# Kernel tuning notes

Measured on AMD Instinct MI355X. Metric: run time of the kernel, lower is better.

The kernel has to match this reference:

```python
import jax, jax.numpy as jnp
import numpy as np

N = 100000   # num_nodes
E = 3200000  # num_edges (avg degree 32)
T = 16       # channels
L = 2        # n_layers


def setup_inputs() -> dict:
    key = jax.random.key(0)
    ks = jax.random.split(key, 6)
    x = jax.random.normal(ks[0], (T, N), dtype=jnp.float32)
    edge_index = jax.random.randint(ks[1], (2, E), 0, N)
    # per-layer scalar params (shared='all' -> shape [1,1] each), init U(-1,1)
    alpha1 = jax.random.uniform(ks[2], (L, 1, 1), minval=-1.0, maxval=1.0, dtype=jnp.float32)
    alpha2 = jax.random.uniform(ks[3], (L, 1, 1), minval=-1.0, maxval=1.0, dtype=jnp.float32)
    gamma = jax.random.uniform(ks[4], (L, 1, 1), minval=-1.0, maxval=1.0, dtype=jnp.float32)
    bias = jax.random.uniform(ks[5], (L, 1, 1), minval=-1.0, maxval=1.0, dtype=jnp.float32)
    return {"x": x, "edge_index": edge_index, "alpha1": alpha1,
            "alpha2": alpha2, "gamma": gamma, "bias": bias}


def reference(x, edge_index, alpha1, alpha2, gamma, bias):
    # DGMRF forward (transpose=False, with_bias=True): stack of L DGMRFLayerMultiChannel
    src, dst = edge_index[0], edge_index[1]
    # degrees = ptg.utils.degree(edge_index[0]) (out-degree of source nodes)
    deg = jax.ops.segment_sum(jnp.ones(E, dtype=x.dtype), src, num_segments=N)
    log_deg = jnp.log(deg)[None, :]          # [1, N]
    edge_log_deg = log_deg[0, dst][None, :]  # [1, E] = log_degrees[edge_index[1]] (non-transpose)
    for l in range(L):
        dp = jax.nn.sigmoid(gamma[l])        # degree_power, [1,1]
        sw = jnp.exp(alpha1[l])              # self_weight
        # NOTE: source's alpha2 property returns alpha1_param when shared != 'dynamics'
        nw = sw * jnp.tanh(alpha1[l])        # neighbor_weight
        weighted_repr = x * jnp.exp(dp * log_deg)        # [T, N]
        ew = jnp.exp((dp - 1.0) * edge_log_deg)          # [1, E] (base edge_weights are ones)
        msg = x[:, src] * ew                              # gather + weight: [T, E]
        agg = jnp.zeros_like(x).at[:, dst].add(msg)       # scatter-add aggregate
        x = sw * weighted_repr + nw * agg + bias[l]
    return x
```

## Files before the change

kernel.cpp:

```cpp
#include <hip/hip_runtime.h>


#define TCH 16
#define BBITS 8
#define BINW (1 << BBITS)
#define BLK 256

typedef int   v4i __attribute__((ext_vector_type(4)));
typedef int   v2i __attribute__((ext_vector_type(2)));
typedef float v4f __attribute__((ext_vector_type(4)));
typedef unsigned int v2u __attribute__((ext_vector_type(2)));

__device__ __forceinline__ float4 bf4_to_f4(uint2 v) {
    float4 f;
    f.x = __uint_as_float(v.x << 16);
    f.y = __uint_as_float(v.x & 0xFFFF0000u);
    f.z = __uint_as_float(v.y << 16);
    f.w = __uint_as_float(v.y & 0xFFFF0000u);
    return f;
}
__device__ __forceinline__ unsigned rne_bf16(float f) {
    unsigned u = __float_as_uint(f);
    return (u + 0x7FFFu + ((u >> 16) & 1u)) >> 16;
}
__device__ __forceinline__ unsigned pack_bf2(float a, float b) {
    return rne_bf16(a) | (rne_bf16(b) << 16);
}

__global__ void k_histtin(const int* __restrict__ src, const int* __restrict__ dst,
                          int* __restrict__ Hd, int* __restrict__ Hs,
                          const float* __restrict__ x, float* __restrict__ xtf,
                          unsigned short* __restrict__ xtb,
                          int E, int N, int NB, int CHUNK, int NBLK) {
    extern __shared__ int sm[];
    int* cd = sm; int* cs2 = sm + NB;
    int t = threadIdx.x;
    if (blockIdx.x < (unsigned)NBLK) {
        for (int i = t; i < 2 * NB; i += BLK) sm[i] = 0;
        __syncthreads();
        int beg = blockIdx.x * CHUNK;
        int end = beg + CHUNK; if (end > E) end = E;
        for (int i = beg + t; i < end; i += BLK) {
            atomicAdd(&cd[dst[i] >> BBITS], 1);
            atomicAdd(&cs2[src[i] >> BBITS], 1);
        }
        __syncthreads();
        int* hd = Hd + (size_t)blockIdx.x * NB;
        int* hs = Hs + (size_t)blockIdx.x * NB;
        for (int b = t; b < NB; b += BLK) { hd[b] = cd[b]; hs[b] = cs2[b]; }
    }
    int n = blockIdx.x * BLK + t;
    if (n < N) {
        float v[TCH];
#pragma unroll
        for (int c = 0; c < TCH; ++c) v[c] = x[(size_t)c * N + n];
        float4* o = reinterpret_cast<float4*>(xtf + (size_t)n * TCH);
        o[0] = make_float4(v[0],  v[1],  v[2],  v[3]);
        o[1] = make_float4(v[4],  v[5],  v[6],  v[7]);
        o[2] = make_float4(v[8],  v[9],  v[10], v[11]);
        o[3] = make_float4(v[12], v[13], v[14], v[15]);
        uint4* ob = reinterpret_cast<uint4*>(xtb + (size_t)n * TCH);
        ob[0] = make_uint4(pack_bf2(v[0], v[1]),  pack_bf2(v[2], v[3]),
                           pack_bf2(v[4], v[5]),  pack_bf2(v[6], v[7]));
        ob[1] = make_uint4(pack_bf2(v[8], v[9]),  pack_bf2(v[10], v[11]),
                           pack_bf2(v[12], v[13]), pack_bf2(v[14], v[15]));
    }
}

__global__ void k_scan2(int* __restrict__ Hd, int* __restrict__ Hs,
                        int* __restrict__ cntd, int* __restrict__ cnts,
                        int NB, int NBLK) {
    __shared__ int ss[BLK];
    int which = (blockIdx.x >= (unsigned)NB) ? 1 : 0;
    int bin = blockIdx.x - which * NB;
    int* H   = which ? Hs : Hd;
    int* cnt = which ? cnts : cntd;
    int t = threadIdx.x;
    int v[4];
    int sum = 0;
#pragma unroll
    for (int j = 0; j < 4; ++j) {
        int b = t * 4 + j;
        v[j] = (b < NBLK) ? H[(size_t)b * NB + bin] : 0;
        sum += v[j];
    }
    ss[t] = sum;
    __syncthreads();
    for (int o = 1; o < BLK; o <<= 1) {
        int u = (t >= o) ? ss[t - o] : 0;
        __syncthreads();
        ss[t] += u;
        __syncthreads();
    }
    int base = ss[t] - sum;
#pragma unroll
    for (int j = 0; j < 4; ++j) {
        int b = t * 4 + j;
        if (b < NBLK) H[(size_t)b * NB + bin] = base;
        base += v[j];
    }
    if (t == BLK - 1) cnt[bin] = ss[BLK - 1];
}

__global__ __launch_bounds__(BLK) void k_place(
        const int* __restrict__ src, const int* __restrict__ dst,
        const int* __restrict__ offd, const int* __restrict__ offs,
        int* __restrict__ dpairs, unsigned char* __restrict__ srcb,
        int E, int NB, int CHUNK, int CAPB) {
    __shared__ int ss[BLK];
    extern __shared__ int sm[];
    int* cur = sm;
    int* gdl = sm + NB;
    int* pay = sm + 2 * NB;
    unsigned short* bino = (unsigned short*)(sm + 2 * NB + CHUNK);

    int t = threadIdx.x;
    int beg = blockIdx.x * CHUNK;
    int end = beg + CHUNK; if (end > E) end = E;
    int m = end - beg;

    for (int i = t; i < NB; i += BLK) cur[i] = 0;
    __syncthreads();
    for (int i = beg + t; i < end; i += BLK)
        atomicAdd(&cur[dst[i] >> BBITS], 1);
    __syncthreads();
    int c0 = (2 * t     < NB) ? cur[2 * t]     : 0;
    int c1 = (2 * t + 1 < NB) ? cur[2 * t + 1] : 0;
    ss[t] = c0 + c1;
    __syncthreads();
    for (int o = 1; o < BLK; o <<= 1) {
        int v = (t >= o) ? ss[t - o] : 0;
        __syncthreads();
        ss[t] += v;
        __syncthreads();
    }
    int excl = ss[t] - (c0 + c1);
    __syncthreads();
    if (2 * t < NB) {
        int od = offd[(size_t)blockIdx.x * NB + 2 * t];
        cur[2 * t] = excl;
        gdl[2 * t] = 2 * t * CAPB + od - excl;
    }
    if (2 * t + 1 < NB) {
        int od = offd[(size_t)blockIdx.x * NB + 2 * t + 1];
        cur[2 * t + 1] = excl + c0;
        gdl[2 * t + 1] = (2 * t + 1) * CAPB + od - (excl + c0);
    }
    __syncthreads();
    for (int i = beg + t; i < end; i += BLK) {
        int d = dst[i], s = src[i];
        int bd = d >> BBITS;
        int ls = atomicAdd(&cur[bd], 1);
        int g  = gdl[bd] + ls;
        if (g < (bd + 1) * CAPB) {
            pay[ls] = ((d & (BINW - 1)) << 24) | s;
            bino[ls] = (unsigned short)bd;
        } else {
            bino[ls] = 0xFFFFu;
        }
    }
    __syncthreads();
    for (int i = t; i < m; i += BLK) {
        int bd = bino[i];
        if (bd != 0xFFFF) dpairs[gdl[bd] + i] = pay[i];
    }
    __syncthreads();

    unsigned char* payb = (unsigned char*)pay;
    for (int i = t; i < NB; i += BLK) cur[i] = 0;
    __syncthreads();
    for (int i = beg + t; i < end; i += BLK)
        atomicAdd(&cur[src[i] >> BBITS], 1);
    __syncthreads();
    c0 = (2 * t     < NB) ? cur[2 * t]     : 0;
    c1 = (2 * t + 1 < NB) ? cur[2 * t + 1] : 0;
    ss[t] = c0 + c1;
    __syncthreads();
    for (int o = 1; o < BLK; o <<= 1) {
        int v = (t >= o) ? ss[t - o] : 0;
        __syncthreads();
        ss[t] += v;
        __syncthreads();
    }
    excl = ss[t] - (c0 + c1);
    __syncthreads();
    if (2 * t < NB) {
        int os_ = offs[(size_t)blockIdx.x * NB + 2 * t];
        cur[2 * t] = excl;
        gdl[2 * t] = 2 * t * CAPB + os_ - excl;
    }
    if (2 * t + 1 < NB) {
        int os_ = offs[(size_t)blockIdx.x * NB + 2 * t + 1];
        cur[2 * t + 1] = excl + c0;
        gdl[2 * t + 1] = (2 * t + 1) * CAPB + os_ - (excl + c0);
    }
    __syncthreads();
    for (int i = beg + t; i < end; i += BLK) {
        int s = src[i];
        int bs = s >> BBITS;
        int ls = atomicAdd(&cur[bs], 1);
        int g  = gdl[bs] + ls;
        if (g < (bs + 1) * CAPB) {
            payb[ls] = (unsigned char)(s & (BINW - 1));
            bino[ls] = (unsigned short)bs;
        } else {
            bino[ls] = 0xFFFFu;
        }
    }
    __syncthreads();
    for (int i = t; i < m; i += BLK) {
        int bs = bino[i];
        if (bs != 0xFFFF) srcb[gdl[bs] + i] = payb[i];
    }
}

__global__ __launch_bounds__(BLK) void k_binsort(
        const int* __restrict__ dpairs, const int* __restrict__ cntd,
        const unsigned char* __restrict__ srcb, const int* __restrict__ cnts,
        int* __restrict__ adj, int2* __restrict__ rc, int* __restrict__ deg,
        int N, int CAPB) {
    __shared__ int h[BINW];
    __shared__ int o[BINW];
    __shared__ int rk[BINW];
    __shared__ int hd[BINW];
    extern __shared__ int lbuf[];
    int bin = blockIdx.x;
    int t = threadIdx.x;
    h[t] = 0; rk[t] = 0; hd[t] = 0;
    __syncthreads();
    int m = cntd[bin]; if (m > CAPB) m = CAPB;
    const int* pp = dpairs + (size_t)bin * CAPB;
    for (int i = t; i < m; i += BLK)
        atomicAdd(&h[((unsigned)pp[i]) >> 24], 1);
    int ms = cnts[bin]; if (ms > CAPB) ms = CAPB;
    const unsigned char* sp = srcb + (size_t)bin * CAPB;
    for (int i = t; i < ms; i += BLK)
        atomicAdd(&hd[sp[i]], 1);
    __syncthreads();
    o[t] = h[t];
    __syncthreads();
    for (int s = 1; s < BINW; s <<= 1) {
        int v = 0;
        if (t >= s) v = o[t - s];
        __syncthreads();
        if (t >= s) o[t] += v;
        __syncthreads();
    }
    int binbase = bin * CAPB;
    {
        int excl = o[t] - h[t];
        o[t] = excl;
        int n = (bin << BBITS) + t;
        if (n < N) { rc[n] = make_int2(binbase + excl, h[t]); deg[n] = hd[t]; }
    }
    __syncthreads();
    for (int i = t; i < m; i += BLK) {
        int w = pp[i];
        int dl = ((unsigned)w) >> 24;
        int s  = w & 0xFFFFFF;
        int r = atomicAdd(&rk[dl], 1);
        lbuf[o[dl] + r] = s;
    }
    __syncthreads();
    for (int i = t; i < m; i += BLK)
        adj[binbase + i] = lbuf[i];
}

__global__ void k_layer(const float* __restrict__ xinf,
                        const unsigned short* __restrict__ xinb,
                        float* __restrict__ xoutf, unsigned short* __restrict__ xoutb,
                        const int2* __restrict__ rc, const int* __restrict__ adj,
                        const int* __restrict__ deg,
                        const float* __restrict__ a1p, const float* __restrict__ gp,
                        const float* __restrict__ bp, int l, int N,
                        int last, float* __restrict__ out) {
    int tt = blockIdx.x * blockDim.x + threadIdx.x;
    int n = tt >> 2;
    int q = tt & 3;
    if (n >= N) return;
    float a1 = a1p[l], g = gp[l], bi = bp[l];
    float dp = 1.0f / (1.0f + expf(-g));
    float sw = expf(a1);
    float nw = sw * tanhf(a1);

    v2i bm = __builtin_nontemporal_load(reinterpret_cast<const v2i*>(rc) + n);
    int b = bm.x, m = bm.y;
    const int* row = adj + b;
    float4 acc0 = make_float4(0.f, 0.f, 0.f, 0.f);
    float4 acc1 = make_float4(0.f, 0.f, 0.f, 0.f);

    int pre = (4 - (b & 3)) & 3; if (pre > m) pre = m;
    int i = 0;
    for (; i < pre; ++i) {
        int s0 = row[i];
        float4 x0 = bf4_to_f4(reinterpret_cast<const uint2*>(xinb + (size_t)s0 * TCH)[q]);
        acc0.x += x0.x; acc0.y += x0.y; acc0.z += x0.z; acc0.w += x0.w;
    }
    const v4i* row4 = reinterpret_cast<const v4i*>(row + pre);
    int nv = (m - pre) >> 2;
    int j = 0;
    for (; j + 1 < nv; j += 2) {
        v4i a4 = __builtin_nontemporal_load(row4 + j);
        v4i b4 = __builtin_nontemporal_load(row4 + j + 1);
        uint2 v0 = reinterpret_cast<const uint2*>(xinb + (size_t)a4.x * TCH)[q];
        uint2 v1 = reinterpret_cast<const uint2*>(xinb + (size_t)a4.y * TCH)[q];
        uint2 v2 = reinterpret_cast<const uint2*>(xinb + (size_t)a4.z * TCH)[q];
        uint2 v3 = reinterpret_cast<const uint2*>(xinb + (size_t)a4.w * TCH)[q];
        uint2 v4 = reinterpret_cast<const uint2*>(xinb + (size_t)b4.x * TCH)[q];
        uint2 v5 = reinterpret_cast<const uint2*>(xinb + (size_t)b4.y * TCH)[q];
        uint2 v6 = reinterpret_cast<const uint2*>(xinb + (size_t)b4.z * TCH)[q];
        uint2 v7 = reinterpret_cast<const uint2*>(xinb + (size_t)b4.w * TCH)[q];
        float4 x0 = bf4_to_f4(v0), x1 = bf4_to_f4(v1), x2 = bf4_to_f4(v2), x3 = bf4_to_f4(v3);
        float4 x4 = bf4_to_f4(v4), x5 = bf4_to_f4(v5), x6 = bf4_to_f4(v6), x7 = bf4_to_f4(v7);
        acc0.x += x0.x; acc0.y += x0.y; acc0.z += x0.z; acc0.w += x0.w;
        acc1.x += x1.x; acc1.y += x1.y; acc1.z += x1.z; acc1.w += x1.w;
        acc0.x += x2.x; acc0.y += x2.y; acc0.z += x2.z; acc0.w += x2.w;
        acc1.x += x3.x; acc1.y += x3.y; acc1.z += x3.z; acc1.w += x3.w;
        acc0.x += x4.x; acc0.y += x4.y; acc0.z += x4.z; acc0.w += x4.w;
        acc1.x += x5.x; acc1.y += x5.y; acc1.z += x5.z; acc1.w += x5.w;
        acc0.x += x6.x; acc0.y += x6.y; acc0.z += x6.z; acc0.w += x6.w;
        acc1.x += x7.x; acc1.y += x7.y; acc1.z += x7.z; acc1.w += x7.w;
    }
    for (; j < nv; ++j) {
        v4i a4 = __builtin_nontemporal_load(row4 + j);
        uint2 v0 = reinterpret_cast<const uint2*>(xinb + (size_t)a4.x * TCH)[q];
        uint2 v1 = reinterpret_cast<const uint2*>(xinb + (size_t)a4.y * TCH)[q];
        uint2 v2 = reinterpret_cast<const uint2*>(xinb + (size_t)a4.z * TCH)[q];
        uint2 v3 = reinterpret_cast<const uint2*>(xinb + (size_t)a4.w * TCH)[q];
        float4 x0 = bf4_to_f4(v0), x1 = bf4_to_f4(v1), x2 = bf4_to_f4(v2), x3 = bf4_to_f4(v3);
        acc0.x += x0.x; acc0.y += x0.y; acc0.z += x0.z; acc0.w += x0.w;
        acc1.x += x1.x; acc1.y += x1.y; acc1.z += x1.z; acc1.w += x1.w;
        acc0.x += x2.x; acc0.y += x2.y; acc0.z += x2.z; acc0.w += x2.w;
        acc1.x += x3.x; acc1.y += x3.y; acc1.z += x3.z; acc1.w += x3.w;
    }
    for (i = pre + (nv << 2); i < m; ++i) {
        int s0 = row[i];
        float4 x0 = bf4_to_f4(reinterpret_cast<const uint2*>(xinb + (size_t)s0 * TCH)[q]);
        acc0.x += x0.x; acc0.y += x0.y; acc0.z += x0.z; acc0.w += x0.w;
    }
    acc0.x += acc1.x; acc0.y += acc1.y; acc0.z += acc1.z; acc0.w += acc1.w;

    float ldg = logf((float)__builtin_nontemporal_load(deg + n));
    float cs = sw * expf(dp * ldg);
    float cn = nw * expf((dp - 1.0f) * ldg);

    v4f xq = __builtin_nontemporal_load(
        reinterpret_cast<const v4f*>(xinf + (size_t)n * TCH) + q);
    float4 r;
    r.x = cs * xq.x + cn * acc0.x + bi;
    r.y = cs * xq.y + cn * acc0.y + bi;
    r.z = cs * xq.z + cn * acc0.z + bi;
    r.w = cs * xq.w + cn * acc0.w + bi;

    if (last) {
        int t0 = q * 4;
        __builtin_nontemporal_store(r.x, out + (size_t)(t0 + 0) * N + n);
        __builtin_nontemporal_store(r.y, out + (size_t)(t0 + 1) * N + n);
        __builtin_nontemporal_store(r.z, out + (size_t)(t0 + 2) * N + n);
        __builtin_nontemporal_store(r.w, out + (size_t)(t0 + 3) * N + n);
    } else {
        v4f rf; rf.x = r.x; rf.y = r.y; rf.z = r.z; rf.w = r.w;
        __builtin_nontemporal_store(rf,
            reinterpret_cast<v4f*>(xoutf + (size_t)n * TCH) + q);
        v2u w2; w2.x = pack_bf2(r.x, r.y); w2.y = pack_bf2(r.z, r.w);
        __builtin_nontemporal_store(w2,
            reinterpret_cast<v2u*>(xoutb + (size_t)n * TCH) + q);
    }
}

extern "C" void kernel_launch(void* const* d_in, const int* in_sizes, int n_in,
                              void* d_out, int out_size, void* d_ws, size_t ws_size,
                              hipStream_t stream) {
    const float* x      = (const float*)d_in[0];
    const int*   ei     = (const int*)d_in[1];
    const float* alpha1 = (const float*)d_in[2];
    const float* gamma  = (const float*)d_in[4];
    const float* bias   = (const float*)d_in[5];
    float* out = (float*)d_out;

    const int N = in_sizes[0] / TCH;
    const int E = in_sizes[1] / 2;
    const int L = in_sizes[2];
    const int* src = ei;
    const int* dst = ei + E;

    const int NB = (N + BINW - 1) >> BBITS;
    int CHUNK = 4096;
    int NBLK = (E + CHUNK - 1) / CHUNK;
    while (NBLK > 4 * BLK) { CHUNK *= 2; NBLK = (E + CHUNK - 1) / CHUNK; }

    auto align = [](size_t v) { return (v + 255) & ~(size_t)255; };
    char* ws = (char*)d_ws;
    size_t off = 0;
    int*  deg   = (int*)(ws + off);  off += align((size_t)N * 4);
    int2* rc    = (int2*)(ws + off); off += align((size_t)N * 8);
    int*  cntd  = (int*)(ws + off);  off += align((size_t)NB * 4);
    int*  cnts  = (int*)(ws + off);  off += align((size_t)NB * 4);
    int*  Hd    = (int*)(ws + off);  off += align((size_t)NBLK * NB * 4);
    int*  Hs    = (int*)(ws + off);  off += align((size_t)NBLK * NB * 4);
    float* xtf0 = (float*)(ws + off); off += align((size_t)N * TCH * 4);
    float* xtf1 = (float*)(ws + off); off += align((size_t)N * TCH * 4);
    unsigned short* xtb0 = (unsigned short*)(ws + off); off += align((size_t)N * TCH * 2);
    unsigned short* xtb1 = (unsigned short*)(ws + off); off += align((size_t)N * TCH * 2);
    long long avg = ((long long)E * BINW + N - 1) / N;
    int CAPB = (int)(avg + avg / 8 + 128);
    size_t rem = (ws_size > off) ? (ws_size - off) : 0;
    size_t cap_fit = rem / ((size_t)NB * 9 + 8);
    if ((size_t)CAPB > cap_fit) CAPB = (int)cap_fit;
    if (CAPB < 4) CAPB = 4;
    if (CAPB > 30000) CAPB = 30000;
    CAPB &= ~3;
    int* dpairs = (int*)(ws + off); off += align((size_t)NB * CAPB * 4);
    int* adj    = (int*)(ws + off); off += align((size_t)NB * CAPB * 4);
    unsigned char* srcb = (unsigned char*)(ws + off);

    dim3 b(BLK);
    int gNn = (N + BLK - 1) / BLK;
    int gHist = (NBLK > gNn) ? NBLK : gNn;
    dim3 gN4(((size_t)N * 4 + BLK - 1) / BLK);

    size_t hist_lds  = (size_t)2 * NB * 4;
    size_t place_lds = (size_t)2 * NB * 4 + (size_t)CHUNK * 4 + (size_t)CHUNK * 2;
    size_t sort_lds  = (size_t)CAPB * 4;

    k_histtin<<<dim3(gHist), b, hist_lds,  stream>>>(src, dst, Hd, Hs, x, xtf0, xtb0,
                                                     E, N, NB, CHUNK, NBLK);
    k_scan2  <<<dim3(2 * NB), b, 0,        stream>>>(Hd, Hs, cntd, cnts, NB, NBLK);
    k_place  <<<dim3(NBLK), b, place_lds,  stream>>>(src, dst, Hd, Hs, dpairs, srcb,
                                                     E, NB, CHUNK, CAPB);
    k_binsort<<<dim3(NB),   b, sort_lds,   stream>>>(dpairs, cntd, srcb, cnts,
                                                     adj, rc, deg, N, CAPB);

    float* xinf = xtf0; float* xof = xtf1;
    unsigned short* xinb = xtb0; unsigned short* xob = xtb1;
    for (int l = 0; l < L; ++l) {
        int last = (l == L - 1) ? 1 : 0;
        k_layer<<<gN4, b, 0, stream>>>(xinf, xinb, xof, xob, rc, adj, deg,
                                       alpha1, gamma, bias, l, N, last, out);
        float* tf = xinf; xinf = xof; xof = tf;
        unsigned short* tb = xinb; xinb = xob; xob = tb;
    }
}
```

Before: 175.5 us.

## Split neighbor list across 4 lanes with full-row gathers and shuffle reduction

The gather kernel previously had each of the 4 lanes per node walk the whole neighbor list and load its own 8-byte channel slice per neighbor. Now each lane takes every 4th neighbor and loads the full 32-byte bf16 row as two 16-byte loads, accumulating all 16 channels. A two-step xor-shuffle reduction then gives each lane its 4 channels. This cuts redundant index reads and uses wider, fewer gather transactions, at the cost of more accumulator registers, cross-lane shuffles, and the loss of the vectorized nontemporal index loads.

```diff
diff --git a/kernel.cpp b/kernel.cpp
--- a/kernel.cpp
+++ b/kernel.cpp
@@ -6,17 +6,16 @@
 #define BINW (1 << BBITS)
 #define BLK 256
 
-typedef int   v4i __attribute__((ext_vector_type(4)));
 typedef int   v2i __attribute__((ext_vector_type(2)));
 typedef float v4f __attribute__((ext_vector_type(4)));
 typedef unsigned int v2u __attribute__((ext_vector_type(2)));
 
-__device__ __forceinline__ float4 bf4_to_f4(uint2 v) {
+__device__ __forceinline__ float4 bf4_to_f4(unsigned lo, unsigned hi) {
     float4 f;
-    f.x = __uint_as_float(v.x << 16);
-    f.y = __uint_as_float(v.x & 0xFFFF0000u);
-    f.z = __uint_as_float(v.y << 16);
-    f.w = __uint_as_float(v.y & 0xFFFF0000u);
+    f.x = __uint_as_float(lo << 16);
+    f.y = __uint_as_float(lo & 0xFFFF0000u);
+    f.z = __uint_as_float(hi << 16);
+    f.w = __uint_as_float(hi & 0xFFFF0000u);
     return f;
 }
 __device__ __forceinline__ unsigned rne_bf16(float f) {
@@ -25,6 +24,25 @@
 }
 __device__ __forceinline__ unsigned pack_bf2(float a, float b) {
     return rne_bf16(a) | (rne_bf16(b) << 16);
+}
+__device__ __forceinline__ float4 shfl_xor4(float4 v, int mask) {
+    float4 r;
+    r.x = __shfl_xor(v.x, mask);
+    r.y = __shfl_xor(v.y, mask);
+    r.z = __shfl_xor(v.z, mask);
+    r.w = __shfl_xor(v.w, mask);
+    return r;
+}
+__device__ __forceinline__ void acc_row(float4& c0, float4& c1, float4& c2, float4& c3,
+                                        uint4 u0, uint4 u1) {
+    float4 x0 = bf4_to_f4(u0.x, u0.y);
+    float4 x1 = bf4_to_f4(u0.z, u0.w);
+    float4 x2 = bf4_to_f4(u1.x, u1.y);
+    float4 x3 = bf4_to_f4(u1.z, u1.w);
+    c0.x += x0.x; c0.y += x0.y; c0.z += x0.z; c0.w += x0.w;
+    c1.x += x1.x; c1.y += x1.y; c1.z += x1.z; c1.w += x1.w;
+    c2.x += x2.x; c2.y += x2.y; c2.z += x2.z; c2.w += x2.w;
+    c3.x += x3.x; c3.y += x3.y; c3.z += x3.z; c3.w += x3.w;
 }
 
 __global__ void k_histtin(const int* __restrict__ src, const int* __restrict__ dst,
@@ -286,59 +304,44 @@
     v2i bm = __builtin_nontemporal_load(reinterpret_cast<const v2i*>(rc) + n);
     int b = bm.x, m = bm.y;
     const int* row = adj + b;
-    float4 acc0 = make_float4(0.f, 0.f, 0.f, 0.f);
-    float4 acc1 = make_float4(0.f, 0.f, 0.f, 0.f);
-
-    int pre = (4 - (b & 3)) & 3; if (pre > m) pre = m;
-    int i = 0;
-    for (; i < pre; ++i) {
+
+    float4 c0 = make_float4(0.f, 0.f, 0.f, 0.f);
+    float4 c1 = make_float4(0.f, 0.f, 0.f, 0.f);
+    float4 c2 = make_float4(0.f, 0.f, 0.f, 0.f);
+    float4 c3 = make_float4(0.f, 0.f, 0.f, 0.f);
+
+    int i = q;
+    for (; i + 4 < m; i += 8) {
         int s0 = row[i];
-        float4 x0 = bf4_to_f4(reinterpret_cast<const uint2*>(xinb + (size_t)s0 * TCH)[q]);
-        acc0.x += x0.x; acc0.y += x0.y; acc0.z += x0.z; acc0.w += x0.w;
-    }
-    const v4i* row4 = reinterpret_cast<const v4i*>(row + pre);
-    int nv = (m - pre) >> 2;
-    int j = 0;
-    for (; j + 1 < nv; j += 2) {
-        v4i a4 = __builtin_nontemporal_load(row4 + j);
-        v4i b4 = __builtin_nontemporal_load(row4 + j + 1);
-        uint2 v0 = reinterpret_cast<const uint2*>(xinb + (size_t)a4.x * TCH)[q];
-        uint2 v1 = reinterpret_cast<const uint2*>(xinb + (size_t)a4.y * TCH)[q];
-        uint2 v2 = reinterpret_cast<const uint2*>(xinb + (size_t)a4.z * TCH)[q];
-        uint2 v3 = reinterpret_cast<const uint2*>(xinb + (size_t)a4.w * TCH)[q];
-        uint2 v4 = reinterpret_cast<const uint2*>(xinb + (size_t)b4.x * TCH)[q];
-        uint2 v5 = reinterpret_cast<const uint2*>(xinb + (size_t)b4.y * TCH)[q];
-        uint2 v6 = reinterpret_cast<const uint2*>(xinb + (size_t)b4.z * TCH)[q];
-        uint2 v7 = reinterpret_cast<const uint2*>(xinb + (size_t)b4.w * TCH)[q];
-        float4 x0 = bf4_to_f4(v0), x1 = bf4_to_f4(v1), x2 = bf4_to_f4(v2), x3 = bf4_to_f4(v3);
-        float4 x4 = bf4_to_f4(v4), x5 = bf4_to_f4(v5), x6 = bf4_to_f4(v6), x7 = bf4_to_f4(v7);
-        acc0.x += x0.x; acc0.y += x0.y; acc0.z += x0.z; acc0.w += x0.w;
-        acc1.x += x1.x; acc1.y += x1.y; acc1.z += x1.z; acc1.w += x1.w;
-        acc0.x += x2.x; acc0.y += x2.y; acc0.z += x2.z; acc0.w += x2.w;
-        acc1.x += x3.x; acc1.y += x3.y; acc1.z += x3.z; acc1.w += x3.w;
-        acc0.x += x4.x; acc0.y += x4.y; acc0.z += x4.z; acc0.w += x4.w;
-        acc1.x += x5.x; acc1.y += x5.y; acc1.z += x5.z; acc1.w += x5.w;
-        acc0.x += x6.x; acc0.y += x6.y; acc0.z += x6.z; acc0.w += x6.w;
-        acc1.x += x7.x; acc1.y += x7.y; acc1.z += x7.z; acc1.w += x7.w;
-    }
-    for (; j < nv; ++j) {
-        v4i a4 = __builtin_nontemporal_load(row4 + j);
-        uint2 v0 = reinterpret_cast<const uint2*>(xinb + (size_t)a4.x * TCH)[q];
-        uint2 v1 = reinterpret_cast<const uint2*>(xinb + (size_t)a4.y * TCH)[q];
-        uint2 v2 = reinterpret_cast<const uint2*>(xinb + (size_t)a4.z * TCH)[q];
-        uint2 v3 = reinterpret_cast<const uint2*>(xinb + (size_t)a4.w * TCH)[q];
-        float4 x0 = bf4_to_f4(v0), x1 = bf4_to_f4(v1), x2 = bf4_to_f4(v2), x3 = bf4_to_f4(v3);
-        acc0.x += x0.x; acc0.y += x0.y; acc0.z += x0.z; acc0.w += x0.w;
-        acc1.x += x1.x; acc1.y += x1.y; acc1.z += x1.z; acc1.w += x1.w;
-        acc0.x += x2.x; acc0.y += x2.y; acc0.z += x2.z; acc0.w += x2.w;
-        acc1.x += x3.x; acc1.y += x3.y; acc1.z += x3.z; acc1.w += x3.w;
-    }
-    for (i = pre + (nv << 2); i < m; ++i) {
+        int s1 = row[i + 4];
+        const uint4* p0 = reinterpret_cast<const uint4*>(xinb + (size_t)s0 * TCH);
+        const uint4* p1 = reinterpret_cast<const uint4*>(xinb + (size_t)s1 * TCH);
+        uint4 a0 = p0[0], a1v = p0[1];
+        uint4 b0 = p1[0], b1v = p1[1];
+        acc_row(c0, c1, c2, c3, a0, a1v);
+        acc_row(c0, c1, c2, c3, b0, b1v);
+    }
+    for (; i < m; i += 4) {
         int s0 = row[i];
-        float4 x0 = bf4_to_f4(reinterpret_cast<const uint2*>(xinb + (size_t)s0 * TCH)[q]);
-        acc0.x += x0.x; acc0.y += x0.y; acc0.z += x0.z; acc0.w += x0.w;
-    }
-    acc0.x += acc1.x; acc0.y += acc1.y; acc0.z += acc1.z; acc0.w += acc1.w;
+        const uint4* p0 = reinterpret_cast<const uint4*>(xinb + (size_t)s0 * TCH);
+        uint4 a0 = p0[0], a1v = p0[1];
+        acc_row(c0, c1, c2, c3, a0, a1v);
+    }
+
+    bool hi = (q & 2) != 0;
+    float4 ka = hi ? c2 : c0;
+    float4 kb = hi ? c3 : c1;
+    float4 sa = hi ? c0 : c2;
+    float4 sb = hi ? c1 : c3;
+    sa = shfl_xor4(sa, 2);
+    sb = shfl_xor4(sb, 2);
+    ka.x += sa.x; ka.y += sa.y; ka.z += sa.z; ka.w += sa.w;
+    kb.x += sb.x; kb.y += sb.y; kb.z += sb.z; kb.w += sb.w;
+    bool lo = (q & 1) != 0;
+    float4 kp = lo ? kb : ka;
+    float4 sp = lo ? ka : kb;
+    sp = shfl_xor4(sp, 1);
+    kp.x += sp.x; kp.y += sp.y; kp.z += sp.z; kp.w += sp.w;
 
     float ldg = logf((float)__builtin_nontemporal_load(deg + n));
     float cs = sw * expf(dp * ldg);
@@ -347,10 +350,10 @@
     v4f xq = __builtin_nontemporal_load(
         reinterpret_cast<const v4f*>(xinf + (size_t)n * TCH) + q);
     float4 r;
-    r.x = cs * xq.x + cn * acc0.x + bi;
-    r.y = cs * xq.y + cn * acc0.y + bi;
-    r.z = cs * xq.z + cn * acc0.z + bi;
-    r.w = cs * xq.w + cn * acc0.w + bi;
+    r.x = cs * xq.x + cn * kp.x + bi;
+    r.y = cs * xq.y + cn * kp.y + bi;
+    r.z = cs * xq.z + cn * kp.z + bi;
+    r.w = cs * xq.w + cn * kp.w + bi;
 
     if (last) {
         int t0 = q * 4;
```

Measured after the change: 159.9 us. -8.9%, faster.
